# Kernel tuning notes

Measured on AMD Instinct MI355X. Metric: run time of the kernel, lower is better.

Reference implementation:

```python
import jax, jax.numpy as jnp
import numpy as np
from jax.ops import segment_sum

N_NODES = 100000


def _gcn_norm(src, dst, n):
    # add self-loops, compute symmetric normalization deg^-1/2 * deg^-1/2
    loop = jnp.arange(n, dtype=src.dtype)
    src_sl = jnp.concatenate([src, loop])
    dst_sl = jnp.concatenate([dst, loop])
    deg = segment_sum(jnp.ones_like(src_sl, dtype=jnp.float32), dst_sl, num_segments=n)
    dinv = jnp.where(deg > 0, jax.lax.rsqrt(deg), 0.0)
    norm = dinv[src_sl] * dinv[dst_sl]  # [E+N]
    return src_sl, dst_sl, norm


def _gcn_conv(x, W, b, src_sl, dst_sl, norm, n):
    h = x @ W                              # [N, out]  dense GEMM first (smaller msg dim)
    msg = h[src_sl] * norm[:, None]        # [E+N, out]
    out = segment_sum(msg, dst_sl, num_segments=n)
    return out + b


def setup_inputs() -> dict:
    key = jax.random.key(0)
    k1, k2, k3, k4, k5 = jax.random.split(key, 5)
    x = jax.random.normal(k1, (N_NODES, 400), dtype=jnp.float32)
    edge_index = jax.random.randint(k2, (2, 3200000), 0, N_NODES, dtype=jnp.int64)
    batch = jnp.zeros((N_NODES,), dtype=jnp.int64)
    # Glorot-style init like PyG GCNConv
    W1 = jax.random.normal(k3, (400, 128), dtype=jnp.float32) * (1.0 / np.sqrt(400))
    b1 = jnp.zeros((128,), dtype=jnp.float32)
    W2 = jax.random.normal(k4, (128, 128), dtype=jnp.float32) * (1.0 / np.sqrt(128))
    b2 = jnp.zeros((128,), dtype=jnp.float32)
    return {"x": x, "edge_index": edge_index, "batch": batch,
            "W1": W1, "b1": b1, "W2": W2, "b2": b2}


def reference(x, edge_index, batch, W1, b1, W2, b2):
    n = x.shape[0]
    src, dst = edge_index[0], edge_index[1]
    src_sl, dst_sl, norm = _gcn_norm(src, dst, n)
    h = jax.nn.relu(_gcn_conv(x, W1, b1, src_sl, dst_sl, norm, n))
    h = jax.nn.relu(_gcn_conv(h, W2, b2, src_sl, dst_sl, norm, n))
    return h
```

## Files before the change

kernel.cpp:

```cpp
#include <hip/hip_runtime.h>


#define NBMAX 1024
#define HB    128

using u16 = unsigned short;
using u32 = unsigned int;
typedef __attribute__((ext_vector_type(8))) short short8;
typedef __attribute__((ext_vector_type(4))) float f32x4;

__device__ __forceinline__ u16 f2bf(float f) {
    u32 u = __float_as_uint(f);
    u += 0x7fffu + ((u >> 16) & 1u);
    return (u16)(u >> 16);
}
__device__ __forceinline__ u32 pack2(float a, float b) {
    return (u32)f2bf(a) | ((u32)f2bf(b) << 16);
}
__device__ __forceinline__ float bflo(u32 u) { return __uint_as_float(u << 16); }
__device__ __forceinline__ float bfhi(u32 u) { return __uint_as_float(u & 0xffff0000u); }


__global__ __launch_bounds__(256) void k_zero(u32* p, int n) {
    int i = blockIdx.x * 256 + threadIdx.x;
    if (i < n) p[i] = 0u;
}

__global__ __launch_bounds__(256) void k_bucket_hist(const int* __restrict__ dst,
                                                     u32* __restrict__ bcnt,
                                                     int E, int NB) {
    __shared__ u32 hist[NBMAX];
    const int tid = threadIdx.x;
    for (int i = tid; i < NB; i += 256) hist[i] = 0u;
    __syncthreads();
    const int chunk = (E + gridDim.x - 1) / gridDim.x;
    const int e0 = blockIdx.x * chunk;
    const int e1 = min(E, e0 + chunk);
    for (int i = e0 + tid; i < e1; i += 256)
        atomicAdd(&hist[dst[i] >> 7], 1u);
    __syncthreads();
    for (int i = tid; i < NB; i += 256) {
        const u32 c = hist[i];
        if (c) atomicAdd(&bcnt[i], c);
    }
}

__global__ __launch_bounds__(256) void k_bucket_scan(const u32* __restrict__ bcnt,
                                                     u32* __restrict__ boff,
                                                     u32* __restrict__ bcur,
                                                     int NB, int E) {
    __shared__ u32 lds[256];
    const int t = threadIdx.x;
    const int base = t * 4;
    u32 v0 = 0, v1 = 0, v2 = 0, v3 = 0;
    if (base + 0 < NB) v0 = bcnt[base + 0];
    if (base + 1 < NB) v1 = bcnt[base + 1];
    if (base + 2 < NB) v2 = bcnt[base + 2];
    if (base + 3 < NB) v3 = bcnt[base + 3];
    const u32 s = v0 + v1 + v2 + v3;
    lds[t] = s;
    __syncthreads();
    for (int off = 1; off < 256; off <<= 1) {
        u32 v = lds[t];
        u32 add = (t >= off) ? lds[t - off] : 0u;
        __syncthreads();
        lds[t] = v + add;
        __syncthreads();
    }
    const u32 excl = lds[t] - s;
    const u32 e0 = excl, e1 = e0 + v0, e2 = e1 + v1, e3 = e2 + v2;
    if (base + 0 < NB) { boff[base + 0] = e0; bcur[base + 0] = e0; }
    if (base + 1 < NB) { boff[base + 1] = e1; bcur[base + 1] = e1; }
    if (base + 2 < NB) { boff[base + 2] = e2; bcur[base + 2] = e2; }
    if (base + 3 < NB) { boff[base + 3] = e3; bcur[base + 3] = e3; }
    if (t == 255) boff[NB] = (u32)E;
}

__global__ __launch_bounds__(256) void k_bucket_scatter(const int* __restrict__ src,
                                                        const int* __restrict__ dst,
                                                        u32* __restrict__ bcur,
                                                        int2* __restrict__ ebuf,
                                                        int E, int NB) {
    __shared__ u32 hist[NBMAX];
    __shared__ u32 base[NBMAX];
    const int tid = threadIdx.x;
    for (int i = tid; i < NB; i += 256) hist[i] = 0u;
    __syncthreads();
    const int chunk = (E + gridDim.x - 1) / gridDim.x;
    const int e0 = blockIdx.x * chunk;
    const int e1 = min(E, e0 + chunk);
    for (int i = e0 + tid; i < e1; i += 256)
        atomicAdd(&hist[dst[i] >> 7], 1u);
    __syncthreads();
    for (int i = tid; i < NB; i += 256) {
        const u32 c = hist[i];
        base[i] = c ? atomicAdd(&bcur[i], c) : 0u;
    }
    __syncthreads();
    for (int i = tid; i < NB; i += 256) hist[i] = 0u;
    __syncthreads();
    for (int i = e0 + tid; i < e1; i += 256) {
        const int s = src[i];
        const int d = dst[i];
        const int b = d >> 7;
        const u32 loc = atomicAdd(&hist[b], 1u);
        ebuf[base[b] + loc] = make_int2(s, d);
    }
}

__global__ __launch_bounds__(256) void k_csr_build(const int2* __restrict__ ebuf,
                                                   const u32* __restrict__ boff,
                                                   int* __restrict__ rowptr,
                                                   float* __restrict__ dinv,
                                                   int* __restrict__ csr_s,
                                                   int N, int NB, int E) {
    __shared__ u32 cnt128[128];
    __shared__ u32 scan128[128];
    __shared__ u32 cur128[128];
    const int tid = threadIdx.x;
    const int b = blockIdx.x;
    const int r0 = (int)boff[b];
    const int r1 = (int)boff[b + 1];

    if (tid < 128) cnt128[tid] = 0u;
    __syncthreads();
    for (int i = r0 + tid; i < r1; i += 256)
        atomicAdd(&cnt128[ebuf[i].y & 127], 1u);
    __syncthreads();

    if (tid < 128) scan128[tid] = cnt128[tid];
    __syncthreads();
    for (int off = 1; off < 128; off <<= 1) {
        u32 v = 0;
        if (tid < 128) {
            v = scan128[tid];
            if (tid >= off) v += scan128[tid - off];
        }
        __syncthreads();
        if (tid < 128) scan128[tid] = v;
        __syncthreads();
    }

    if (tid < 128) {
        const u32 deg  = cnt128[tid];
        const u32 excl = scan128[tid] - deg;
        cur128[tid] = excl;
        const int node = b * 128 + tid;
        if (node < N) {
            rowptr[node] = r0 + (int)excl;
            dinv[node]   = rsqrtf((float)(deg + 1u));
        }
    }
    if (b == 0 && tid == 0) rowptr[N] = E;
    __syncthreads();

    for (int i = r0 + tid; i < r1; i += 256) {
        const int2 e = ebuf[i];
        const u32 p = atomicAdd(&cur128[e.y & 127], 1u);
        csr_s[r0 + (int)p] = e.x;
    }
}

__global__ __launch_bounds__(256) void k_wprep(const float* __restrict__ W,
                                               u16* __restrict__ Wt,
                                               int K, int KP) {
    int idx = blockIdx.x * 256 + threadIdx.x;
    if (idx >= 128 * KP) return;
    int n = idx / KP, k = idx - n * KP;
    Wt[idx] = (k < K) ? f2bf(W[(size_t)k * 128 + n]) : (u16)0;
}

template <int ABF>
__global__ __launch_bounds__(512) void k_gemm_mfma(
        const void* __restrict__ Aptr,
        const u16* __restrict__ Wt,
        u16* __restrict__ H, int M, int K, int KP) {
    __shared__ u16 smem[16384];
    u16* As = smem;
    u16* Bs = smem + 128 * 64;

    const int tid = threadIdx.x;
    const int row0 = blockIdx.x * 128;
    const int wid = tid >> 6;
    const int lane = tid & 63;
    const int wm = wid >> 2, wn = wid & 3;
    const int l15 = lane & 15, lg = lane >> 4;
    const int lr7 = l15 & 7;

    const int arow = tid >> 2;
    const int achk = tid & 3;
    const int grow = row0 + arow;
    const int ar7 = arow & 7;
    const int s0 = (achk * 2) ^ ar7;
    const int s1 = (achk * 2 + 1) ^ ar7;

    float4 ar0, ar1, ar2, ar3;
    uint4  au0, au1;
    uint4  bu0, bu1;

    auto load_tile = [&](int kt) {
        const int k0 = kt * 64 + achk * 16;
        if (ABF) {
            if (grow < M) {
                const u16* ap = (const u16*)Aptr + (size_t)grow * K + k0;
                au0 = *reinterpret_cast<const uint4*>(ap);
                au1 = *reinterpret_cast<const uint4*>(ap + 8);
            } else {
                au0 = make_uint4(0, 0, 0, 0);
                au1 = make_uint4(0, 0, 0, 0);
            }
        } else {
            if (grow < M && k0 < K) {
                const float* ap = (const float*)Aptr + (size_t)grow * K + k0;
                ar0 = *reinterpret_cast<const float4*>(ap);
                ar1 = *reinterpret_cast<const float4*>(ap + 4);
                ar2 = *reinterpret_cast<const float4*>(ap + 8);
                ar3 = *reinterpret_cast<const float4*>(ap + 12);
            } else {
                ar0 = ar1 = ar2 = ar3 = make_float4(0.f, 0.f, 0.f, 0.f);
            }
        }
        const u16* wp = Wt + (size_t)arow * KP + k0;
        bu0 = *reinterpret_cast<const uint4*>(wp);
        bu1 = *reinterpret_cast<const uint4*>(wp + 8);
    };

    auto store_tile = [&]() {
        uint4 w0, w1;
        if (ABF) {
            w0 = au0; w1 = au1;
        } else {
            w0.x = pack2(ar0.x, ar0.y); w0.y = pack2(ar0.z, ar0.w);
            w0.z = pack2(ar1.x, ar1.y); w0.w = pack2(ar1.z, ar1.w);
            w1.x = pack2(ar2.x, ar2.y); w1.y = pack2(ar2.z, ar2.w);
            w1.z = pack2(ar3.x, ar3.y); w1.w = pack2(ar3.z, ar3.w);
        }
        u16* ad = As + arow * 64;
        *reinterpret_cast<uint4*>(ad + s0 * 8) = w0;
        *reinterpret_cast<uint4*>(ad + s1 * 8) = w1;
        u16* bd = Bs + arow * 64;
        *reinterpret_cast<uint4*>(bd + s0 * 8) = bu0;
        *reinterpret_cast<uint4*>(bd + s1 * 8) = bu1;
    };

    f32x4 acc[4][2];
#pragma unroll
    for (int i = 0; i < 4; ++i)
#pragma unroll
        for (int j = 0; j < 2; ++j)
            acc[i][j] = (f32x4){0.f, 0.f, 0.f, 0.f};

    const int NT = KP >> 6;
    load_tile(0);
    for (int kt = 0; kt < NT; ++kt) {
        __syncthreads();
        store_tile();
        __syncthreads();
        if (kt + 1 < NT) load_tile(kt + 1);
#pragma unroll
        for (int sub = 0; sub < 2; ++sub) {
            const int slot = ((sub * 4 + lg) ^ lr7) * 8;
            short8 af[4], bf[2];
#pragma unroll
            for (int i = 0; i < 4; ++i)
                af[i] = *reinterpret_cast<const short8*>(
                    As + (wm * 64 + i * 16 + l15) * 64 + slot);
#pragma unroll
            for (int j = 0; j < 2; ++j)
                bf[j] = *reinterpret_cast<const short8*>(
                    Bs + (wn * 32 + j * 16 + l15) * 64 + slot);
#pragma unroll
            for (int i = 0; i < 4; ++i)
#pragma unroll
                for (int j = 0; j < 2; ++j)
                    acc[i][j] = __builtin_amdgcn_mfma_f32_16x16x32_bf16(
                        af[i], bf[j], acc[i][j], 0, 0, 0);
        }
    }

    const int CSTR = 136;
    __syncthreads();
#pragma unroll
    for (int half = 0; half < 2; ++half) {
        if (wm == half) {
#pragma unroll
            for (int i = 0; i < 4; ++i)
#pragma unroll
                for (int j = 0; j < 2; ++j)
#pragma unroll
                    for (int r = 0; r < 4; ++r)
                        smem[(i * 16 + lg * 4 + r) * CSTR + wn * 32 + j * 16 + l15] =
                            f2bf(acc[i][j][r]);
        }
        __syncthreads();
        {
            const int rr = tid >> 3;
            const int cc = (tid & 7) * 16;
            const int gr = row0 + half * 64 + rr;
            if (gr < M) {
                const u16* cp = smem + rr * CSTR + cc;
                uint4 q0 = *reinterpret_cast<const uint4*>(cp);
                uint4 q1 = *reinterpret_cast<const uint4*>(cp + 8);
                uint4* hp = reinterpret_cast<uint4*>(H + (size_t)gr * 128 + cc);
                hp[0] = q0; hp[1] = q1;
            }
        }
        __syncthreads();
    }
}

template <int OUTBF>
__global__ __launch_bounds__(256) void k_gather(const int* __restrict__ rowptr,
                                                const int* __restrict__ csr_s,
                                                const float* __restrict__ dinv,
                                                const u16* __restrict__ H,
                                                const float* __restrict__ bias,
                                                void* __restrict__ outp, int N) {
    const int t = threadIdx.x;
    const int node = blockIdx.x * 16 + (t >> 4);
    if (node >= N) return;
    const int lane = t & 15;
    const int c8 = lane * 8;

    const float dv = dinv[node];
    const uint4 hv = *reinterpret_cast<const uint4*>(H + (size_t)node * 128 + c8);
    float acc0 = dv * bflo(hv.x), acc1 = dv * bfhi(hv.x);
    float acc2 = dv * bflo(hv.y), acc3 = dv * bfhi(hv.y);
    float acc4 = dv * bflo(hv.z), acc5 = dv * bfhi(hv.z);
    float acc6 = dv * bflo(hv.w), acc7 = dv * bfhi(hv.w);

    const int beg = rowptr[node], end = rowptr[node + 1];
    for (int r = beg; r < end; r += 16) {
        const int cntc = min(16, end - r);
        int sv = (lane < cntc) ? csr_s[r + lane] : 0;
        for (int j = 0; j < cntc; ++j) {
            const int s = __shfl(sv, j, 16);
            const float w = dinv[s];
            const uint4 x = *reinterpret_cast<const uint4*>(H + (size_t)s * 128 + c8);
            acc0 = fmaf(w, bflo(x.x), acc0); acc1 = fmaf(w, bfhi(x.x), acc1);
            acc2 = fmaf(w, bflo(x.y), acc2); acc3 = fmaf(w, bfhi(x.y), acc3);
            acc4 = fmaf(w, bflo(x.z), acc4); acc5 = fmaf(w, bfhi(x.z), acc5);
            acc6 = fmaf(w, bflo(x.w), acc6); acc7 = fmaf(w, bfhi(x.w), acc7);
        }
    }

    const float4 b0 = *reinterpret_cast<const float4*>(bias + c8);
    const float4 b1 = *reinterpret_cast<const float4*>(bias + c8 + 4);
    const float r0 = fmaxf(fmaf(acc0, dv, b0.x), 0.f);
    const float r1 = fmaxf(fmaf(acc1, dv, b0.y), 0.f);
    const float r2 = fmaxf(fmaf(acc2, dv, b0.z), 0.f);
    const float r3 = fmaxf(fmaf(acc3, dv, b0.w), 0.f);
    const float r4 = fmaxf(fmaf(acc4, dv, b1.x), 0.f);
    const float r5 = fmaxf(fmaf(acc5, dv, b1.y), 0.f);
    const float r6 = fmaxf(fmaf(acc6, dv, b1.z), 0.f);
    const float r7 = fmaxf(fmaf(acc7, dv, b1.w), 0.f);

    if (OUTBF) {
        uint4 q;
        q.x = pack2(r0, r1); q.y = pack2(r2, r3);
        q.z = pack2(r4, r5); q.w = pack2(r6, r7);
        u16* op = (u16*)outp + (size_t)node * 128 + c8;
        *reinterpret_cast<uint4*>(op) = q;
    } else {
        float* op = (float*)outp + (size_t)node * 128 + c8;
        *reinterpret_cast<float4*>(op)     = make_float4(r0, r1, r2, r3);
        *reinterpret_cast<float4*>(op + 4) = make_float4(r4, r5, r6, r7);
    }
}


extern "C" void kernel_launch(void* const* d_in, const int* in_sizes, int n_in,
                              void* d_out, int out_size, void* d_ws, size_t ws_size,
                              hipStream_t stream) {
    const float* x  = (const float*)d_in[0];
    const int*   ei = (const int*)d_in[1];
    const float* W1 = (const float*)d_in[3];
    const float* b1 = (const float*)d_in[4];
    const float* W2 = (const float*)d_in[5];
    const float* b2 = (const float*)d_in[6];
    float* out = (float*)d_out;

    const int N = in_sizes[0] / 400;
    const int E = in_sizes[1] / 2;
    const int* src = ei;
    const int* dst = ei + E;
    const int NB = (N + 127) >> 7;
    const int KP1 = 448;
    const int KP2 = 128;

    char* ws = (char*)d_ws;
    size_t off = 0;
    auto alloc = [&](size_t bytes) {
        void* p = ws + off;
        off = (off + bytes + 255) & ~(size_t)255;
        return p;
    };
    u32*   bcnt   = (u32*)alloc((size_t)NB * 4);
    u32*   boff   = (u32*)alloc((size_t)(NB + 1) * 4);
    u32*   bcur   = (u32*)alloc((size_t)NB * 4);
    int*   rowptr = (int*)alloc((size_t)(N + 1) * 4);
    float* dinv   = (float*)alloc((size_t)N * 4);
    int*   csr_s  = (int*)alloc((size_t)E * 4);
    u16*   h      = (u16*)alloc((size_t)N * 128 * 2);
    u16*   abf    = (u16*)alloc((size_t)N * 128 * 2);
    int2*  ebuf   = (int2*)alloc((size_t)E * 8);
    u16*   Wt1    = (u16*)alloc((size_t)128 * KP1 * 2);
    u16*   Wt2    = (u16*)alloc((size_t)128 * KP2 * 2);

    const int nb_gm = (N + 127) / 128;
    const int nb_g  = (N + 15) / 16;

    k_wprep<<<(128 * KP1 + 255) / 256, 256, 0, stream>>>(W1, Wt1, 400, KP1);
    k_wprep<<<(128 * KP2 + 255) / 256, 256, 0, stream>>>(W2, Wt2, 128, KP2);

    k_zero<<<(NB + 255) / 256, 256, 0, stream>>>(bcnt, NB);
    k_bucket_hist<<<HB, 256, 0, stream>>>(dst, bcnt, E, NB);
    k_bucket_scan<<<1, 256, 0, stream>>>(bcnt, boff, bcur, NB, E);
    k_bucket_scatter<<<HB, 256, 0, stream>>>(src, dst, bcur, ebuf, E, NB);
    k_csr_build<<<NB, 256, 0, stream>>>(ebuf, boff, rowptr, dinv, csr_s, N, NB, E);

    k_gemm_mfma<0><<<nb_gm, 512, 0, stream>>>(x, Wt1, h, N, 400, KP1);
    k_gather<1><<<nb_g, 256, 0, stream>>>(rowptr, csr_s, dinv, h, b1, abf, N);

    k_gemm_mfma<1><<<nb_gm, 512, 0, stream>>>(abf, Wt2, h, N, 128, KP2);
    k_gather<0><<<nb_g, 256, 0, stream>>>(rowptr, csr_s, dinv, h, b2, out, N);
}
```

Measured before the change: 457.3 us.

## Slice H into 16-column panels and pre-scale rows by dinv in GEMM epilogue

The GEMM epilogue now multiplies each output row by dinv and writes H in a sliced layout of 8 panels of 16 columns ([8][N][16]). The gather kernel handles one panel per block group, with 4 lanes per node, and drops the per-edge dinv[s] lookup. Each panel (about 3.2 MB) is small enough to stay cache-resident during the random gathers. The cost is that the CSR indices are read 8 times, there are more blocks, and each load is a narrower 8-byte access.

```diff
diff --git a/kernel.cpp b/kernel.cpp
--- a/kernel.cpp
+++ b/kernel.cpp
@@ -174,6 +174,7 @@
 __global__ __launch_bounds__(512) void k_gemm_mfma(
         const void* __restrict__ Aptr,
         const u16* __restrict__ Wt,
+        const float* __restrict__ dinv,
         u16* __restrict__ H, int M, int K, int KP) {
     __shared__ u16 smem[16384];
     u16* As = smem;
@@ -202,7 +203,8 @@
         const int k0 = kt * 64 + achk * 16;
         if (ABF) {
             if (grow < M) {
-                const u16* ap = (const u16*)Aptr + (size_t)grow * K + k0;
+                const u16* ap = (const u16*)Aptr + (size_t)(k0 >> 4) * M * 16
+                                + (size_t)grow * 16;
                 au0 = *reinterpret_cast<const uint4*>(ap);
                 au1 = *reinterpret_cast<const uint4*>(ap + 8);
             } else {
@@ -286,23 +288,27 @@
 #pragma unroll
             for (int i = 0; i < 4; ++i)
 #pragma unroll
-                for (int j = 0; j < 2; ++j)
-#pragma unroll
-                    for (int r = 0; r < 4; ++r)
+                for (int r = 0; r < 4; ++r) {
+                    const int gr = row0 + half * 64 + i * 16 + lg * 4 + r;
+                    const float dv = (gr < M) ? dinv[gr] : 0.f;
+#pragma unroll
+                    for (int j = 0; j < 2; ++j)
                         smem[(i * 16 + lg * 4 + r) * CSTR + wn * 32 + j * 16 + l15] =
-                            f2bf(acc[i][j][r]);
+                            f2bf(acc[i][j][r] * dv);
+                }
         }
         __syncthreads();
         {
             const int rr = tid >> 3;
-            const int cc = (tid & 7) * 16;
+            const int p  = tid & 7;
             const int gr = row0 + half * 64 + rr;
             if (gr < M) {
-                const u16* cp = smem + rr * CSTR + cc;
+                const u16* cp = smem + rr * CSTR + p * 16;
                 uint4 q0 = *reinterpret_cast<const uint4*>(cp);
                 uint4 q1 = *reinterpret_cast<const uint4*>(cp + 8);
-                uint4* hp = reinterpret_cast<uint4*>(H + (size_t)gr * 128 + cc);
-                hp[0] = q0; hp[1] = q1;
+                u16* hp = H + (size_t)p * M * 16 + (size_t)gr * 16;
+                *reinterpret_cast<uint4*>(hp)     = q0;
+                *reinterpret_cast<uint4*>(hp + 8) = q1;
             }
         }
         __syncthreads();
@@ -313,58 +319,49 @@
 __global__ __launch_bounds__(256) void k_gather(const int* __restrict__ rowptr,
                                                 const int* __restrict__ csr_s,
                                                 const float* __restrict__ dinv,
-                                                const u16* __restrict__ H,
+                                                const u16* __restrict__ Hs,
                                                 const float* __restrict__ bias,
                                                 void* __restrict__ outp, int N) {
-    const int t = threadIdx.x;
-    const int node = blockIdx.x * 16 + (t >> 4);
+    const int pass = blockIdx.x & 7;
+    const int g    = blockIdx.x >> 3;
+    const int t    = threadIdx.x;
+    const int node = g * 64 + (t >> 2);
     if (node >= N) return;
-    const int lane = t & 15;
-    const int c8 = lane * 8;
+    const int lane = t & 3;
+    const u16* __restrict__ HS = Hs + (size_t)pass * N * 16;
 
     const float dv = dinv[node];
-    const uint4 hv = *reinterpret_cast<const uint4*>(H + (size_t)node * 128 + c8);
-    float acc0 = dv * bflo(hv.x), acc1 = dv * bfhi(hv.x);
-    float acc2 = dv * bflo(hv.y), acc3 = dv * bfhi(hv.y);
-    float acc4 = dv * bflo(hv.z), acc5 = dv * bfhi(hv.z);
-    float acc6 = dv * bflo(hv.w), acc7 = dv * bfhi(hv.w);
+    const uint2 hv = *reinterpret_cast<const uint2*>(HS + (size_t)node * 16 + lane * 4);
+    float a0 = bflo(hv.x), a1 = bfhi(hv.x), a2 = bflo(hv.y), a3 = bfhi(hv.y);
 
     const int beg = rowptr[node], end = rowptr[node + 1];
-    for (int r = beg; r < end; r += 16) {
-        const int cntc = min(16, end - r);
+    for (int r = beg; r < end; r += 4) {
+        const int cntc = min(4, end - r);
         int sv = (lane < cntc) ? csr_s[r + lane] : 0;
         for (int j = 0; j < cntc; ++j) {
-            const int s = __shfl(sv, j, 16);
-            const float w = dinv[s];
-            const uint4 x = *reinterpret_cast<const uint4*>(H + (size_t)s * 128 + c8);
-            acc0 = fmaf(w, bflo(x.x), acc0); acc1 = fmaf(w, bfhi(x.x), acc1);
-            acc2 = fmaf(w, bflo(x.y), acc2); acc3 = fmaf(w, bfhi(x.y), acc3);
-            acc4 = fmaf(w, bflo(x.z), acc4); acc5 = fmaf(w, bfhi(x.z), acc5);
-            acc6 = fmaf(w, bflo(x.w), acc6); acc7 = fmaf(w, bfhi(x.w), acc7);
-        }
-    }
-
-    const float4 b0 = *reinterpret_cast<const float4*>(bias + c8);
-    const float4 b1 = *reinterpret_cast<const float4*>(bias + c8 + 4);
-    const float r0 = fmaxf(fmaf(acc0, dv, b0.x), 0.f);
-    const float r1 = fmaxf(fmaf(acc1, dv, b0.y), 0.f);
-    const float r2 = fmaxf(fmaf(acc2, dv, b0.z), 0.f);
-    const float r3 = fmaxf(fmaf(acc3, dv, b0.w), 0.f);
-    const float r4 = fmaxf(fmaf(acc4, dv, b1.x), 0.f);
-    const float r5 = fmaxf(fmaf(acc5, dv, b1.y), 0.f);
-    const float r6 = fmaxf(fmaf(acc6, dv, b1.z), 0.f);
-    const float r7 = fmaxf(fmaf(acc7, dv, b1.w), 0.f);
+            const int s = __shfl(sv, j, 4);
+            const uint2 xv = *reinterpret_cast<const uint2*>(HS + (size_t)s * 16 + lane * 4);
+            a0 += bflo(xv.x); a1 += bfhi(xv.x);
+            a2 += bflo(xv.y); a3 += bfhi(xv.y);
+        }
+    }
+
+    const int cbase = pass * 16 + lane * 4;
+    const float4 bb = *reinterpret_cast<const float4*>(bias + cbase);
+    const float r0 = fmaxf(fmaf(a0, dv, bb.x), 0.f);
+    const float r1 = fmaxf(fmaf(a1, dv, bb.y), 0.f);
+    const float r2 = fmaxf(fmaf(a2, dv, bb.z), 0.f);
+    const float r3 = fmaxf(fmaf(a3, dv, bb.w), 0.f);
 
     if (OUTBF) {
-        uint4 q;
-        q.x = pack2(r0, r1); q.y = pack2(r2, r3);
-        q.z = pack2(r4, r5); q.w = pack2(r6, r7);
-        u16* op = (u16*)outp + (size_t)node * 128 + c8;
-        *reinterpret_cast<uint4*>(op) = q;
+        u16* op = (u16*)outp + (size_t)pass * N * 16 + (size_t)node * 16 + lane * 4;
+        uint2 q;
+        q.x = pack2(r0, r1);
+        q.y = pack2(r2, r3);
+        *reinterpret_cast<uint2*>(op) = q;
     } else {
-        float* op = (float*)outp + (size_t)node * 128 + c8;
-        *reinterpret_cast<float4*>(op)     = make_float4(r0, r1, r2, r3);
-        *reinterpret_cast<float4*>(op + 4) = make_float4(r4, r5, r6, r7);
+        float* op = (float*)outp + (size_t)node * 128 + cbase;
+        *reinterpret_cast<float4*>(op) = make_float4(r0, r1, r2, r3);
     }
 }
 
@@ -401,14 +398,14 @@
     int*   rowptr = (int*)alloc((size_t)(N + 1) * 4);
     float* dinv   = (float*)alloc((size_t)N * 4);
     int*   csr_s  = (int*)alloc((size_t)E * 4);
-    u16*   h      = (u16*)alloc((size_t)N * 128 * 2);
+    u16*   hs     = (u16*)alloc((size_t)N * 128 * 2);
     u16*   abf    = (u16*)alloc((size_t)N * 128 * 2);
     int2*  ebuf   = (int2*)alloc((size_t)E * 8);
     u16*   Wt1    = (u16*)alloc((size_t)128 * KP1 * 2);
     u16*   Wt2    = (u16*)alloc((size_t)128 * KP2 * 2);
 
     const int nb_gm = (N + 127) / 128;
-    const int nb_g  = (N + 15) / 16;
+    const int nb_g  = 8 * ((N + 63) / 64);
 
     k_wprep<<<(128 * KP1 + 255) / 256, 256, 0, stream>>>(W1, Wt1, 400, KP1);
     k_wprep<<<(128 * KP2 + 255) / 256, 256, 0, stream>>>(W2, Wt2, 128, KP2);
@@ -419,9 +416,9 @@
     k_bucket_scatter<<<HB, 256, 0, stream>>>(src, dst, bcur, ebuf, E, NB);
     k_csr_build<<<NB, 256, 0, stream>>>(ebuf, boff, rowptr, dinv, csr_s, N, NB, E);
 
-    k_gemm_mfma<0><<<nb_gm, 512, 0, stream>>>(x, Wt1, h, N, 400, KP1);
-    k_gather<1><<<nb_g, 256, 0, stream>>>(rowptr, csr_s, dinv, h, b1, abf, N);
-
-    k_gemm_mfma<1><<<nb_gm, 512, 0, stream>>>(abf, Wt2, h, N, 128, KP2);
-    k_gather<0><<<nb_g, 256, 0, stream>>>(rowptr, csr_s, dinv, h, b2, out, N);
-}
+    k_gemm_mfma<0><<<nb_gm, 512, 0, stream>>>(x, Wt1, dinv, hs, N, 400, KP1);
+    k_gather<1><<<nb_g, 256, 0, stream>>>(rowptr, csr_s, dinv, hs, b1, abf, N);
+
+    k_gemm_mfma<1><<<nb_gm, 512, 0, stream>>>(abf, Wt2, dinv, hs, N, 128, KP2);
+    k_gather<0><<<nb_g, 256, 0, stream>>>(rowptr, csr_s, dinv, hs, b2, out, N);
+}
```

Measured after the change: 641.2 us. +40.2%, slower.
